# Performance work log

Measured on AMD Instinct MI355X. Metric: run time of the kernel, lower is better.

## Reference

```python
import jax, jax.numpy as jnp
import numpy as np

N = 20000      # nodes
E = 320000     # edges (avg degree 16)
DIN, H1, H2, DOUT = 256, 256, 128, 64


def _lin_params(key, din, dout):
    kw, kb = jax.random.split(key)
    s = 1.0 / np.sqrt(din)
    W = jax.random.uniform(kw, (din, dout), jnp.float32, -s, s)
    b = jax.random.uniform(kb, (dout,), jnp.float32, -s, s)
    return W, b


def setup_inputs() -> dict:
    key = jax.random.key(0)
    keys = jax.random.split(key, 20)
    inp = {
        'x': jax.random.normal(keys[0], (N, DIN), jnp.float32),
        'edge_index': jax.random.randint(keys[1], (2, E), 0, N, jnp.int64),
    }
    dims = [(DIN, H1), (DIN, H1), (DIN, H1),   # layer1 key/query/value
            (H1, H2), (H1, H2), (H1, H2),      # layer2
            (H2, DOUT), (H2, DOUT), (H2, DOUT)]  # layer3
    names = ['k1', 'q1', 'v1', 'k2', 'q2', 'v2', 'k3', 'q3', 'v3']
    for i, (nm, (di, do)) in enumerate(zip(names, dims)):
        W, b = _lin_params(keys[2 + i], di, do)
        inp[nm + '_w'] = W
        inp[nm + '_b'] = b
    # skip (root) weights, no bias per PyG, plus per-conv output bias
    for j, (di, do) in enumerate([(DIN, H1), (H1, H2), (H2, DOUT)], start=1):
        s = 1.0 / np.sqrt(di)
        inp[f's{j}_w'] = jax.random.uniform(keys[11 + 2 * j], (di, do), jnp.float32, -s, s)
        inp[f'bias{j}'] = jnp.zeros((do,), jnp.float32)
    return inp


def _res_gated_conv(x, src, dst, kw, kb, qw, qb, vw, vb, sw, bias):
    # PyG ResGatedGraphConv (flow source_to_target, aggr='add', act=Sigmoid):
    # out_i = lin_skip(x_i) + sum_{j->i} sigmoid(lin_key(x_i) + lin_query(x_j)) * lin_value(x_j) + bias
    k = x @ kw + kb            # [N, D]
    q = x @ qw + qb
    v = x @ vw + vb
    eta = jax.nn.sigmoid(k[dst] + q[src])   # [E, D] edge gate
    msg = eta * v[src]                      # [E, D]
    agg = jax.ops.segment_sum(msg, dst, num_segments=N)  # scatter-add to targets
    return x @ sw + agg + bias


def reference(x, edge_index,
              k1_w, k1_b, q1_w, q1_b, v1_w, v1_b,
              k2_w, k2_b, q2_w, q2_b, v2_w, v2_b,
              k3_w, k3_b, q3_w, q3_b, v3_w, v3_b,
              s1_w, bias1, s2_w, bias2, s3_w, bias3):
    src, dst = edge_index[0], edge_index[1]
    h = _res_gated_conv(x, src, dst, k1_w, k1_b, q1_w, q1_b, v1_w, v1_b, s1_w, bias1)
    # dropout (eval mode -> identity)
    h = _res_gated_conv(h, src, dst, k2_w, k2_b, q2_w, q2_b, v2_w, v2_b, s2_w, bias2)
    h = _res_gated_conv(h, src, dst, k3_w, k3_b, q3_w, q3_b, v3_w, v3_b, s3_w, bias3)
    return jax.nn.softmax(h, axis=1)
```

## Files before the change

### kernel.cpp

```cpp
#include <hip/hip_runtime.h>
#include <hip/hip_bf16.h>
#include <type_traits>


#define NN 20000
#define EE 320000
#define ELLW 64

typedef _Float16 half8 __attribute__((ext_vector_type(8)));
typedef _Float16 half4 __attribute__((ext_vector_type(4)));
typedef _Float16 half2v __attribute__((ext_vector_type(2)));
typedef float f32x4 __attribute__((ext_vector_type(4)));

__device__ __forceinline__ _Float16 f2h(float f) { return (_Float16)f; }
__device__ __forceinline__ float fsigmoid_mul(float v, float x) {
    return v * __builtin_amdgcn_rcpf(1.f + __expf(-x));
}

struct PrepArgs {
    const float* w[3][4];
    const float* b[3][4];
    _Float16* wt[3];
    float* cb[3];
};

__global__ __launch_bounds__(256) void setup_all_kernel(
    const int* __restrict__ ei, int* __restrict__ deg, int* __restrict__ flag,
    const float* __restrict__ x, _Float16* __restrict__ Xh, PrepArgs a) {
    const int b = blockIdx.x;
    const int tid = threadIdx.x;
    if (b < 79) {
        const int i = b * 256 + tid;
        if (i < NN) deg[i] = 0;
    } else if (b == 79) {
        __shared__ int nz;
        if (tid == 0) nz = 0;
        __syncthreads();
        int c = 0;
        for (int t = tid; t < 1024; t += 256)
            if (ei[2 * t + 1] != 0) c = 1;
        if (c) atomicAdd(&nz, 1);
        __syncthreads();
        if (tid == 0) *flag = (nz == 0) ? 1 : 0;
    } else if (b < 1744) {
        const int idx = (b - 80) * 256 + tid;
        int layer, li, K, D;
        if (idx < 262144) {
            layer = 0; li = idx; K = 256; D = 256;
        } else if (idx < 393216) {
            layer = 1; li = idx - 262144; K = 256; D = 128;
        } else {
            layer = 2; li = idx - 393216; K = 128; D = 64;
        }
        const int p = li / K;
        const int k = li - p * K;
        int grp, c;
        if (p < D) {
            grp = 0; c = p;
        } else if (p < 3 * D) {
            const int t = p - D;
            grp = (t & 1) ? 2 : 1;
            c = t >> 1;
        } else {
            grp = 3; c = p - 3 * D;
        }
        a.wt[layer][(size_t)p * K + k] =
            f2h(a.w[layer][grp][(size_t)k * D + c]);
        if (k == 0) a.cb[layer][p] = a.b[layer][grp][c];
    } else {
        const int i = ((b - 1744) * 256 + tid) * 8;
        if (i < NN * 256) {
            const float4 f0 = *(const float4*)(x + i);
            const float4 f1 = *(const float4*)(x + i + 4);
            half8 h;
            h[0] = f2h(f0.x); h[1] = f2h(f0.y); h[2] = f2h(f0.z); h[3] = f2h(f0.w);
            h[4] = f2h(f1.x); h[5] = f2h(f1.y); h[6] = f2h(f1.z); h[7] = f2h(f1.w);
            *(half8*)(Xh + i) = h;
        }
    }
}

__device__ __forceinline__ void gemm_tile(
    int bm, int bn, const _Float16* __restrict__ A,
    const _Float16* __restrict__ Bt, const float* __restrict__ catbias,
    _Float16* __restrict__ O, int M, int K, int N) {
    __shared__ _Float16 As[2][4096];
    __shared__ _Float16 Bs[2][4096];

    const int tid = threadIdx.x;
    const int wid = tid >> 6;
    const int lane = tid & 63;
    const int tile_m = bm * 128;
    const int tile_n = bn * 128;
    const int wm = (wid & 1) * 64;
    const int wn = (wid >> 1) * 64;

    const int st_row = (wid << 4) + (lane >> 2);
    const int st_kc = (lane & 3) << 3;

    auto stage = [&](int buf, int kt) {
#pragma unroll
        for (int j = 0; j < 2; ++j) {
            int ar = tile_m + j * 64 + st_row;
            ar = ar < M ? ar : M - 1;
            const _Float16* ag = A + (size_t)ar * K + kt + st_kc;
            __builtin_amdgcn_global_load_lds(
                (const __attribute__((address_space(1))) unsigned int*)ag,
                (__attribute__((address_space(3))) unsigned int*)
                    &As[buf][j * 2048 + (wid << 9)],
                16, 0, 0);
            const int br = tile_n + j * 64 + st_row;
            const _Float16* bg = Bt + (size_t)br * K + kt + st_kc;
            __builtin_amdgcn_global_load_lds(
                (const __attribute__((address_space(1))) unsigned int*)bg,
                (__attribute__((address_space(3))) unsigned int*)
                    &Bs[buf][j * 2048 + (wid << 9)],
                16, 0, 0);
        }
    };

    stage(0, 0);

    f32x4 acc[4][4] = {};
    const int fr = lane & 15;
    const int fk = (lane >> 4) << 3;
    const int niter = K >> 5;

    for (int it = 0; it < niter; ++it) {
        __syncthreads();
        if (it + 1 < niter) stage((it + 1) & 1, (it + 1) << 5);
        const _Float16* as = As[it & 1];
        const _Float16* bs = Bs[it & 1];
        half8 af[4], bf[4];
#pragma unroll
        for (int mi = 0; mi < 4; ++mi)
            af[mi] = *(const half8*)&as[(wm + mi * 16 + fr) * 32 + fk];
#pragma unroll
        for (int ni = 0; ni < 4; ++ni)
            bf[ni] = *(const half8*)&bs[(wn + ni * 16 + fr) * 32 + fk];
#pragma unroll
        for (int mi = 0; mi < 4; ++mi)
#pragma unroll
            for (int ni = 0; ni < 4; ++ni)
                acc[mi][ni] = __builtin_amdgcn_mfma_f32_16x16x32_f16(
                    af[mi], bf[ni], acc[mi][ni], 0, 0, 0);
    }
    __syncthreads();

    _Float16* zone = &As[0][0] + wid * 2048;
    const int cl = lane & 15;
    const int rq = (lane >> 4) << 2;
    const int col0 = tile_n + wn;
    const int r0 = tile_m + wm;
#pragma unroll
    for (int mi = 0; mi < 4; ++mi) {
#pragma unroll
        for (int ni = 0; ni < 4; ++ni) {
            const float cb = catbias[col0 + ni * 16 + cl];
#pragma unroll
            for (int r = 0; r < 4; ++r)
                zone[(rq + r) * 72 + ni * 16 + cl] = f2h(acc[mi][ni][r] + cb);
        }
#pragma unroll
        for (int j = 0; j < 2; ++j) {
            const int rr = j * 8 + (lane >> 3);
            const int row = r0 + mi * 16 + rr;
            const half8 v = *(const half8*)&zone[rr * 72 + (lane & 7) * 8];
            if (row < M)
                *(half8*)&O[(size_t)row * N + col0 + (lane & 7) * 8] = v;
        }
    }
}

__global__ __launch_bounds__(256) void gemm_kernel(
    const _Float16* __restrict__ A, const _Float16* __restrict__ Bt,
    const float* __restrict__ catbias, _Float16* __restrict__ O, int M, int K,
    int N, int mblocks) {
    gemm_tile(blockIdx.x % mblocks, blockIdx.x / mblocks, A, Bt, catbias, O, M,
              K, N);
}

__global__ __launch_bounds__(256) void gemm1_fill_kernel(
    const _Float16* __restrict__ A, const _Float16* __restrict__ Bt,
    const float* __restrict__ catbias, _Float16* __restrict__ O,
    const int* __restrict__ ei, const int* __restrict__ i64flag,
    int* __restrict__ deg, unsigned short* __restrict__ col) {
    if (blockIdx.x < 1256) {
        gemm_tile(blockIdx.x % 157, blockIdx.x / 157, A, Bt, catbias, O, NN,
                  256, 1024);
        return;
    }
    const int e = (blockIdx.x - 1256) * 256 + threadIdx.x;
    if (e >= EE) return;
    int src, dst;
    if (*i64flag) {
        const long long* p = (const long long*)ei;
        src = (int)p[e];
        dst = (int)p[EE + e];
    } else {
        src = ei[e];
        dst = ei[EE + e];
    }
    const int pos = atomicAdd(&deg[dst], 1);
    if (pos < ELLW) col[dst * ELLW + pos] = (unsigned short)src;
}

template <int D>
__global__ __launch_bounds__(256) void edge_gather_slice_kernel(
    const int* __restrict__ deg, const unsigned short* __restrict__ col,
    const _Float16* __restrict__ KQVS, _Float16* __restrict__ Hh, int n) {
    constexpr int NSL = D / 32;
    constexpr int D4 = 4 * D;
    const int b = blockIdx.x;
    const int s = b % NSL;
    const int g = b / NSL;
    const int node = g * 4 + (threadIdx.x >> 6);
    if (node >= n) return;
    const int lane = threadIdx.x & 63;
    const int d = lane & 31;
    const int esub = lane >> 5;

    int dg = deg[node];
    dg = dg < ELLW ? dg : ELLW;
    int idx = (int)col[node * ELLW + lane];
    if (lane >= dg) idx = node;

    const int el = s * 32 + d;
    const float k = (float)KQVS[(size_t)node * D4 + el];
    const _Float16* qv = KQVS + D + 2 * el;
    float acc = 0.f;

    for (int e = 0; e < dg; e += 4) {
        const int s0 = __shfl(idx, e + esub, 64);
        const int s1 = __shfl(idx, e + 2 + esub, 64);
        const half2v u0 = *(const half2v*)(qv + (size_t)s0 * D4);
        const half2v u1 = *(const half2v*)(qv + (size_t)s1 * D4);
        const float g0 = fsigmoid_mul((float)u0[1], k + (float)u0[0]);
        acc += (e + esub < dg) ? g0 : 0.f;
        const float g1 = fsigmoid_mul((float)u1[1], k + (float)u1[0]);
        acc += (e + 2 + esub < dg) ? g1 : 0.f;
    }
    acc += __shfl_xor(acc, 32, 64);

    if (lane < 32) {
        const float skip = (float)KQVS[(size_t)node * D4 + 3 * D + el];
        Hh[(size_t)node * D + el] = f2h(skip + acc);
    }
}

template <int D, int MODE>
__global__ __launch_bounds__(256, 4) void edge_gather_kernel(
    const int* __restrict__ deg, const unsigned short* __restrict__ col,
    const _Float16* __restrict__ KQVS, _Float16* __restrict__ Hh,
    float* __restrict__ out, int n) {
    constexpr int DV = D / 64;
    constexpr int D4 = 4 * D;
    using qv_t = typename std::conditional<
        DV == 4, half8,
        typename std::conditional<DV == 2, half4, half2v>::type>::type;

    const int node = blockIdx.x * 4 + (threadIdx.x >> 6);
    if (node >= n) return;
    const int lane = threadIdx.x & 63;
    const int ld = lane * DV;

    int dg = deg[node];
    dg = dg < ELLW ? dg : ELLW;
    int idx = (int)col[node * ELLW + lane];
    if (lane >= dg) idx = node;

    float k[DV], acc[DV];
    {
        const _Float16* kp = KQVS + (size_t)node * D4 + ld;
        if constexpr (DV == 4) {
            const half4 u = *(const half4*)kp;
#pragma unroll
            for (int j = 0; j < 4; ++j) k[j] = (float)u[j];
        } else if constexpr (DV == 2) {
            const half2v u = *(const half2v*)kp;
            k[0] = (float)u[0]; k[1] = (float)u[1];
        } else {
            k[0] = (float)*kp;
        }
    }
#pragma unroll
    for (int j = 0; j < DV; ++j) acc[j] = 0.f;

    auto ldqv = [&](qv_t& u, int e) {
        const int s = __builtin_amdgcn_readlane(idx, e);
        const qv_t* p = (const qv_t*)(KQVS + (size_t)s * D4 + D) + lane;
        u = *p;
    };
    auto edgeacc = [&](qv_t u) {
#pragma unroll
        for (int j = 0; j < DV; ++j)
            acc[j] += fsigmoid_mul((float)u[2 * j + 1], k[j] + (float)u[2 * j]);
    };

    qv_t ua[8], ub[8];
    auto issue = [&](qv_t* u, int e0) {
#pragma unroll
        for (int j = 0; j < 8; ++j) ldqv(u[j], e0 + j);
    };
    auto consume8 = [&](qv_t* u) {
#pragma unroll
        for (int j = 0; j < 8; ++j) edgeacc(u[j]);
    };
    auto consume_tail = [&](qv_t* u, int nb) {
#pragma unroll
        for (int j = 0; j < 8; ++j)
            if (j < nb) edgeacc(u[j]);
    };

    if (dg > 0) {
        issue(ua, 0);
        for (int e = 0;;) {
            int nb = dg - e;
            if (nb <= 8) {
                __builtin_amdgcn_sched_barrier(0);
                consume_tail(ua, nb);
                break;
            }
            issue(ub, e + 8);
            __builtin_amdgcn_sched_barrier(0);
            consume8(ua);
            e += 8;
            nb = dg - e;
            if (nb <= 8) {
                __builtin_amdgcn_sched_barrier(0);
                consume_tail(ub, nb);
                break;
            }
            issue(ua, e + 8);
            __builtin_amdgcn_sched_barrier(0);
            consume8(ub);
            e += 8;
        }
    }

    float h[DV];
    {
        const _Float16* sp = KQVS + (size_t)node * D4 + 3 * D + ld;
        if constexpr (DV == 4) {
            const half4 u = *(const half4*)sp;
#pragma unroll
            for (int j = 0; j < 4; ++j) h[j] = (float)u[j] + acc[j];
        } else if constexpr (DV == 2) {
            const half2v u = *(const half2v*)sp;
            h[0] = (float)u[0] + acc[0];
            h[1] = (float)u[1] + acc[1];
        } else {
            h[0] = (float)*sp + acc[0];
        }
    }

    if constexpr (MODE == 0) {
        _Float16* op = Hh + (size_t)node * D + ld;
        if constexpr (DV == 4) {
            half4 o;
#pragma unroll
            for (int j = 0; j < 4; ++j) o[j] = f2h(h[j]);
            *(half4*)op = o;
        } else if constexpr (DV == 2) {
            half2v o;
            o[0] = f2h(h[0]); o[1] = f2h(h[1]);
            *(half2v*)op = o;
        } else {
            op[0] = f2h(h[0]);
        }
    } else {
        static_assert(MODE == 0 || DV == 1, "softmax fusion needs D==64");
        float m = h[0];
#pragma unroll
        for (int off = 32; off > 0; off >>= 1)
            m = fmaxf(m, __shfl_xor(m, off, 64));
        const float ex = __expf(h[0] - m);
        float sm = ex;
#pragma unroll
        for (int off = 32; off > 0; off >>= 1) sm += __shfl_xor(sm, off, 64);
        out[(size_t)node * 64 + lane] = ex * __builtin_amdgcn_rcpf(sm);
    }
}

extern "C" void kernel_launch(void* const* d_in, const int* in_sizes, int n_in,
                              void* d_out, int out_size, void* d_ws,
                              size_t ws_size, hipStream_t stream) {
    const float* x = (const float*)d_in[0];
    const int* ei = (const int*)d_in[1];

    char* w = (char*)d_ws;
    _Float16* Xh = (_Float16*)w;     w += (size_t)NN * 256 * 2;
    _Float16* KQVS = (_Float16*)w;   w += (size_t)NN * 1024 * 2;
    _Float16* H1h = (_Float16*)w;    w += (size_t)NN * 256 * 2;
    _Float16* H2h = (_Float16*)w;    w += (size_t)NN * 128 * 2;
    _Float16* Wt1 = (_Float16*)w;    w += (size_t)1024 * 256 * 2;
    _Float16* Wt2 = (_Float16*)w;    w += (size_t)512 * 256 * 2;
    _Float16* Wt3 = (_Float16*)w;    w += (size_t)256 * 128 * 2;
    float* cb1 = (float*)w;          w += 1024 * 4;
    float* cb2 = (float*)w;          w += 512 * 4;
    float* cb3 = (float*)w;          w += 256 * 4;
    int* i64flag = (int*)w;          w += 16;
    int* deg = (int*)w;              w += (size_t)NN * 4;
    unsigned short* ell = (unsigned short*)w;  w += (size_t)NN * ELLW * 2;

    const dim3 blk(256);
    const int gblocks = (NN + 3) / 4;

    PrepArgs pa;
    pa.w[0][0] = (const float*)d_in[2];  pa.b[0][0] = (const float*)d_in[3];
    pa.w[0][1] = (const float*)d_in[4];  pa.b[0][1] = (const float*)d_in[5];
    pa.w[0][2] = (const float*)d_in[6];  pa.b[0][2] = (const float*)d_in[7];
    pa.w[1][0] = (const float*)d_in[8];  pa.b[1][0] = (const float*)d_in[9];
    pa.w[1][1] = (const float*)d_in[10]; pa.b[1][1] = (const float*)d_in[11];
    pa.w[1][2] = (const float*)d_in[12]; pa.b[1][2] = (const float*)d_in[13];
    pa.w[2][0] = (const float*)d_in[14]; pa.b[2][0] = (const float*)d_in[15];
    pa.w[2][1] = (const float*)d_in[16]; pa.b[2][1] = (const float*)d_in[17];
    pa.w[2][2] = (const float*)d_in[18]; pa.b[2][2] = (const float*)d_in[19];
    pa.w[0][3] = (const float*)d_in[20]; pa.b[0][3] = (const float*)d_in[21];
    pa.w[1][3] = (const float*)d_in[22]; pa.b[1][3] = (const float*)d_in[23];
    pa.w[2][3] = (const float*)d_in[24]; pa.b[2][3] = (const float*)d_in[25];
    pa.wt[0] = Wt1; pa.wt[1] = Wt2; pa.wt[2] = Wt3;
    pa.cb[0] = cb1; pa.cb[1] = cb2; pa.cb[2] = cb3;

    setup_all_kernel<<<4244, blk, 0, stream>>>(ei, deg, i64flag, x, Xh, pa);

    gemm1_fill_kernel<<<2506, blk, 0, stream>>>(Xh, Wt1, cb1, KQVS, ei,
                                                i64flag, deg, ell);
    edge_gather_slice_kernel<256><<<gblocks * 8, blk, 0, stream>>>(
        deg, ell, KQVS, H1h, NN);

    gemm_kernel<<<157 * 4, blk, 0, stream>>>(H1h, Wt2, cb2, KQVS, NN, 256, 512,
                                             157);
    edge_gather_slice_kernel<128><<<gblocks * 4, blk, 0, stream>>>(
        deg, ell, KQVS, H2h, NN);

    gemm_kernel<<<157 * 2, blk, 0, stream>>>(H2h, Wt3, cb3, KQVS, NN, 128, 256,
                                             157);
    edge_gather_kernel<64, 1><<<gblocks, blk, 0, stream>>>(
        deg, ell, KQVS, nullptr, (float*)d_out, NN);
}
```

Measured before the change: 287.2 us.

## Reorganize q/v weight interleave and vectorize sliced edge gather with fp16 exp

```diff
diff --git a/kernel.cpp b/kernel.cpp
--- a/kernel.cpp
+++ b/kernel.cpp
@@ -15,6 +15,11 @@
 __device__ __forceinline__ _Float16 f2h(float f) { return (_Float16)f; }
 __device__ __forceinline__ float fsigmoid_mul(float v, float x) {
     return v * __builtin_amdgcn_rcpf(1.f + __expf(-x));
+}
+__device__ __forceinline__ _Float16 h_exp2(_Float16 x) {
+    _Float16 r;
+    asm("v_exp_f16 %0, %1" : "=v"(r) : "v"(x));
+    return r;
 }
 
 struct PrepArgs {
@@ -59,8 +64,14 @@
             grp = 0; c = p;
         } else if (p < 3 * D) {
             const int t = p - D;
-            grp = (t & 1) ? 2 : 1;
-            c = t >> 1;
+            if (layer < 2) {
+                const int pb = t >> 2, r = t & 3;
+                grp = (r < 2) ? 1 : 2;
+                c = 2 * pb + (r & 1);
+            } else {
+                grp = (t & 1) ? 2 : 1;
+                c = t >> 1;
+            }
         } else {
             grp = 3; c = p - 3 * D;
         }
@@ -212,39 +223,111 @@
     constexpr int NSL = D / 32;
     constexpr int D4 = 4 * D;
     const int b = blockIdx.x;
-    const int s = b % NSL;
+    const int sl = b % NSL;
     const int g = b / NSL;
     const int node = g * 4 + (threadIdx.x >> 6);
     if (node >= n) return;
     const int lane = threadIdx.x & 63;
-    const int d = lane & 31;
-    const int esub = lane >> 5;
+    const int d = lane & 7;
+    const int esub = lane >> 3;
 
     int dg = deg[node];
     dg = dg < ELLW ? dg : ELLW;
     int idx = (int)col[node * ELLW + lane];
     if (lane >= dg) idx = node;
 
-    const int el = s * 32 + d;
-    const float k = (float)KQVS[(size_t)node * D4 + el];
-    const _Float16* qv = KQVS + D + 2 * el;
-    float acc = 0.f;
-
-    for (int e = 0; e < dg; e += 4) {
-        const int s0 = __shfl(idx, e + esub, 64);
-        const int s1 = __shfl(idx, e + 2 + esub, 64);
-        const half2v u0 = *(const half2v*)(qv + (size_t)s0 * D4);
-        const half2v u1 = *(const half2v*)(qv + (size_t)s1 * D4);
-        const float g0 = fsigmoid_mul((float)u0[1], k + (float)u0[0]);
-        acc += (e + esub < dg) ? g0 : 0.f;
-        const float g1 = fsigmoid_mul((float)u1[1], k + (float)u1[0]);
-        acc += (e + 2 + esub < dg) ? g1 : 0.f;
-    }
-    acc += __shfl_xor(acc, 32, 64);
-
-    if (lane < 32) {
-        const float skip = (float)KQVS[(size_t)node * D4 + 3 * D + el];
-        Hh[(size_t)node * D + el] = f2h(skip + acc);
+    const half2v mlg = {(_Float16)-1.44269504f, (_Float16)-1.44269504f};
+    const half4 kq =
+        *(const half4*)(KQVS + (size_t)node * D4 + sl * 32 + d * 4);
+    const half2v mk01 = half2v{kq[0], kq[1]} * mlg;
+    const half2v mk23 = half2v{kq[2], kq[3]} * mlg;
+
+    float acc0 = 0.f, acc1 = 0.f, acc2 = 0.f, acc3 = 0.f;
+
+    const _Float16* qv0 = KQVS + D + 64 * sl + 8 * d;
+
+    auto ldqv = [&](half8& u, int e0) {
+        const int s = __shfl(idx, e0 + esub, 64);
+        u = *(const half8*)(qv0 + ((size_t)s << (D == 256 ? 10 : 9)));
+    };
+    auto gate = [&](half8 u, float& g0, float& g1, float& g2, float& g3) {
+        const half2v mt01 = half2v{u[0], u[1]} * mlg + mk01;
+        const half2v mt23 = half2v{u[4], u[5]} * mlg + mk23;
+        const float e0 = (float)h_exp2(mt01[0]);
+        const float e1 = (float)h_exp2(mt01[1]);
+        const float e2 = (float)h_exp2(mt23[0]);
+        const float e3 = (float)h_exp2(mt23[1]);
+        const float r0 = __builtin_amdgcn_rcpf(1.f + e0);
+        const float r1 = __builtin_amdgcn_rcpf(1.f + e1);
+        const float r2 = __builtin_amdgcn_rcpf(1.f + e2);
+        const float r3 = __builtin_amdgcn_rcpf(1.f + e3);
+        g0 = r0 * (float)u[2];
+        g1 = r1 * (float)u[3];
+        g2 = r2 * (float)u[6];
+        g3 = r3 * (float)u[7];
+    };
+    auto consume8 = [&](half8 u) {
+        float g0, g1, g2, g3;
+        gate(u, g0, g1, g2, g3);
+        acc0 += g0; acc1 += g1; acc2 += g2; acc3 += g3;
+    };
+    auto consume_tail = [&](half8 u, int nb) {
+        const float msk = (esub < nb) ? 1.f : 0.f;
+        float g0, g1, g2, g3;
+        gate(u, g0, g1, g2, g3);
+        acc0 += msk * g0; acc1 += msk * g1;
+        acc2 += msk * g2; acc3 += msk * g3;
+    };
+
+    if (dg > 0) {
+        half8 ua, ub;
+        ldqv(ua, 0);
+        for (int e = 0;;) {
+            int nb = dg - e;
+            if (nb <= 8) {
+                __builtin_amdgcn_sched_barrier(0);
+                consume_tail(ua, nb);
+                break;
+            }
+            ldqv(ub, e + 8);
+            __builtin_amdgcn_sched_barrier(0);
+            consume8(ua);
+            e += 8;
+            nb = dg - e;
+            if (nb <= 8) {
+                __builtin_amdgcn_sched_barrier(0);
+                consume_tail(ub, nb);
+                break;
+            }
+            ldqv(ua, e + 8);
+            __builtin_amdgcn_sched_barrier(0);
+            consume8(ub);
+            e += 8;
+        }
+    }
+
+    acc0 += __shfl_xor(acc0, 8, 64);
+    acc0 += __shfl_xor(acc0, 16, 64);
+    acc0 += __shfl_xor(acc0, 32, 64);
+    acc1 += __shfl_xor(acc1, 8, 64);
+    acc1 += __shfl_xor(acc1, 16, 64);
+    acc1 += __shfl_xor(acc1, 32, 64);
+    acc2 += __shfl_xor(acc2, 8, 64);
+    acc2 += __shfl_xor(acc2, 16, 64);
+    acc2 += __shfl_xor(acc2, 32, 64);
+    acc3 += __shfl_xor(acc3, 8, 64);
+    acc3 += __shfl_xor(acc3, 16, 64);
+    acc3 += __shfl_xor(acc3, 32, 64);
+
+    if (esub == 0) {
+        const half4 sv =
+            *(const half4*)(KQVS + (size_t)node * D4 + 3 * D + sl * 32 + d * 4);
+        half4 o;
+        o[0] = f2h((float)sv[0] + acc0);
+        o[1] = f2h((float)sv[1] + acc1);
+        o[2] = f2h((float)sv[2] + acc2);
+        o[3] = f2h((float)sv[3] + acc3);
+        *(half4*)(Hh + (size_t)node * D + sl * 32 + d * 4) = o;
     }
 }
 
```

Result: faster. 275.9 us (-3.9%).

## Interleave KQVS columns per 32-feature slice and pipeline slice gathers

Applied to the files above, without the earlier changes.

```diff
diff --git a/kernel.cpp b/kernel.cpp
--- a/kernel.cpp
+++ b/kernel.cpp
@@ -54,15 +54,17 @@
         }
         const int p = li / K;
         const int k = li - p * K;
+        const int sl = p >> 7;
+        const int r = p & 127;
         int grp, c;
-        if (p < D) {
-            grp = 0; c = p;
-        } else if (p < 3 * D) {
-            const int t = p - D;
+        if (r < 32) {
+            grp = 0; c = sl * 32 + r;
+        } else if (r < 96) {
+            const int t = r - 32;
             grp = (t & 1) ? 2 : 1;
-            c = t >> 1;
+            c = sl * 32 + (t >> 1);
         } else {
-            grp = 3; c = p - 3 * D;
+            grp = 3; c = sl * 32 + (r - 96);
         }
         a.wt[layer][(size_t)p * K + k] =
             f2h(a.w[layer][grp][(size_t)k * D + c]);
@@ -206,107 +208,126 @@
 }
 
 template <int D>
-__global__ __launch_bounds__(256) void edge_gather_slice_kernel(
+__global__ __launch_bounds__(256, 4) void slice_gather_kernel(
     const int* __restrict__ deg, const unsigned short* __restrict__ col,
     const _Float16* __restrict__ KQVS, _Float16* __restrict__ Hh, int n) {
     constexpr int NSL = D / 32;
     constexpr int D4 = 4 * D;
     const int b = blockIdx.x;
-    const int s = b % NSL;
-    const int g = b / NSL;
-    const int node = g * 4 + (threadIdx.x >> 6);
+    const int sl = b % NSL;
+    const int node = (b / NSL) * 4 + (threadIdx.x >> 6);
     if (node >= n) return;
     const int lane = threadIdx.x & 63;
-    const int d = lane & 31;
-    const int esub = lane >> 5;
+    const int fl = lane & 31;
+    const int eh = lane >> 5;
 
     int dg = deg[node];
     dg = dg < ELLW ? dg : ELLW;
     int idx = (int)col[node * ELLW + lane];
     if (lane >= dg) idx = node;
 
-    const int el = s * 32 + d;
-    const float k = (float)KQVS[(size_t)node * D4 + el];
-    const _Float16* qv = KQVS + D + 2 * el;
+    const _Float16* chunk_n = KQVS + (size_t)node * D4 + sl * 128;
+    const float k = (float)chunk_n[fl];
     float acc = 0.f;
 
-    for (int e = 0; e < dg; e += 4) {
-        const int s0 = __shfl(idx, e + esub, 64);
-        const int s1 = __shfl(idx, e + 2 + esub, 64);
-        const half2v u0 = *(const half2v*)(qv + (size_t)s0 * D4);
-        const half2v u1 = *(const half2v*)(qv + (size_t)s1 * D4);
-        const float g0 = fsigmoid_mul((float)u0[1], k + (float)u0[0]);
-        acc += (e + esub < dg) ? g0 : 0.f;
-        const float g1 = fsigmoid_mul((float)u1[1], k + (float)u1[0]);
-        acc += (e + 2 + esub < dg) ? g1 : 0.f;
-    }
+    auto ldqv = [&](half2v& u, int e2) {
+        const int sA = __builtin_amdgcn_readlane(idx, e2);
+        const int sB = __builtin_amdgcn_readlane(idx, e2 + 1);
+        const int s = (lane < 32) ? sA : sB;
+        u = *((const half2v*)(KQVS + (size_t)s * D4 + sl * 128 + 32) + fl);
+    };
+    auto edgeacc = [&](half2v u, float m) {
+        acc += m * fsigmoid_mul((float)u[1], k + (float)u[0]);
+    };
+
+    half2v ua[4], ub[4];
+    auto issue = [&](half2v* u, int e0) {
+#pragma unroll
+        for (int i = 0; i < 4; ++i) ldqv(u[i], e0 + 2 * i);
+    };
+    auto consume4 = [&](half2v* u) {
+#pragma unroll
+        for (int i = 0; i < 4; ++i) edgeacc(u[i], 1.f);
+    };
+    auto consume_tail = [&](half2v* u, int nb) {
+#pragma unroll
+        for (int i = 0; i < 4; ++i) {
+            const float m = (2 * i + eh < nb) ? 1.f : 0.f;
+            edgeacc(u[i], m);
+        }
+    };
+
+    if (dg > 0) {
+        issue(ua, 0);
+        for (int e = 0;;) {
+            int nb = dg - e;
+            if (nb <= 8) {
+                __builtin_amdgcn_sched_barrier(0);
+                consume_tail(ua, nb);
+                break;
+            }
+            issue(ub, e + 8);
+            __builtin_amdgcn_sched_barrier(0);
+            consume4(ua);
+            e += 8;
+            nb = dg - e;
+            if (nb <= 8) {
+                __builtin_amdgcn_sched_barrier(0);
+                consume_tail(ub, nb);
+                break;
+            }
+            issue(ua, e + 8);
+            __builtin_amdgcn_sched_barrier(0);
+            consume4(ub);
+            e += 8;
+        }
+    }
+
     acc += __shfl_xor(acc, 32, 64);
 
     if (lane < 32) {
-        const float skip = (float)KQVS[(size_t)node * D4 + 3 * D + el];
-        Hh[(size_t)node * D + el] = f2h(skip + acc);
-    }
-}
-
-template <int D, int MODE>
-__global__ __launch_bounds__(256, 4) void edge_gather_kernel(
+        const float skip = (float)chunk_n[96 + fl];
+        Hh[(size_t)node * D + sl * 32 + fl] = f2h(skip + acc);
+    }
+}
+
+__global__ __launch_bounds__(256, 4) void gather64_softmax_kernel(
     const int* __restrict__ deg, const unsigned short* __restrict__ col,
-    const _Float16* __restrict__ KQVS, _Float16* __restrict__ Hh,
-    float* __restrict__ out, int n) {
-    constexpr int DV = D / 64;
-    constexpr int D4 = 4 * D;
-    using qv_t = typename std::conditional<
-        DV == 4, half8,
-        typename std::conditional<DV == 2, half4, half2v>::type>::type;
-
+    const _Float16* __restrict__ KQVS, float* __restrict__ out, int n) {
     const int node = blockIdx.x * 4 + (threadIdx.x >> 6);
     if (node >= n) return;
     const int lane = threadIdx.x & 63;
-    const int ld = lane * DV;
+    const int sl = lane >> 5;
+    const int fo = lane & 31;
+    const int qvoff = sl * 128 + 32 + 2 * fo;
 
     int dg = deg[node];
     dg = dg < ELLW ? dg : ELLW;
     int idx = (int)col[node * ELLW + lane];
     if (lane >= dg) idx = node;
 
-    float k[DV], acc[DV];
-    {
-        const _Float16* kp = KQVS + (size_t)node * D4 + ld;
-        if constexpr (DV == 4) {
-            const half4 u = *(const half4*)kp;
-#pragma unroll
-            for (int j = 0; j < 4; ++j) k[j] = (float)u[j];
-        } else if constexpr (DV == 2) {
-            const half2v u = *(const half2v*)kp;
-            k[0] = (float)u[0]; k[1] = (float)u[1];
-        } else {
-            k[0] = (float)*kp;
-        }
-    }
-#pragma unroll
-    for (int j = 0; j < DV; ++j) acc[j] = 0.f;
-
-    auto ldqv = [&](qv_t& u, int e) {
+    const _Float16* chunk_n = KQVS + (size_t)node * 256 + sl * 128;
+    const float k = (float)chunk_n[fo];
+    float acc = 0.f;
+
+    auto ldqv = [&](half2v& u, int e) {
         const int s = __builtin_amdgcn_readlane(idx, e);
-        const qv_t* p = (const qv_t*)(KQVS + (size_t)s * D4 + D) + lane;
-        u = *p;
-    };
-    auto edgeacc = [&](qv_t u) {
-#pragma unroll
-        for (int j = 0; j < DV; ++j)
-            acc[j] += fsigmoid_mul((float)u[2 * j + 1], k[j] + (float)u[2 * j]);
-    };
-
-    qv_t ua[8], ub[8];
-    auto issue = [&](qv_t* u, int e0) {
+        u = *(const half2v*)(KQVS + (size_t)s * 256 + qvoff);
+    };
+    auto edgeacc = [&](half2v u) {
+        acc += fsigmoid_mul((float)u[1], k + (float)u[0]);
+    };
+
+    half2v ua[8], ub[8];
+    auto issue = [&](half2v* u, int e0) {
 #pragma unroll
         for (int j = 0; j < 8; ++j) ldqv(u[j], e0 + j);
     };
-    auto consume8 = [&](qv_t* u) {
+    auto consume8 = [&](half2v* u) {
 #pragma unroll
         for (int j = 0; j < 8; ++j) edgeacc(u[j]);
     };
-    auto consume_tail = [&](qv_t* u, int nb) {
+    auto consume_tail = [&](half2v* u, int nb) {
 #pragma unroll
         for (int j = 0; j < 8; ++j)
             if (j < nb) edgeacc(u[j]);
@@ -338,48 +359,17 @@
         }
     }
 
-    float h[DV];
-    {
-        const _Float16* sp = KQVS + (size_t)node * D4 + 3 * D + ld;
-        if constexpr (DV == 4) {
-            const half4 u = *(const half4*)sp;
-#pragma unroll
-            for (int j = 0; j < 4; ++j) h[j] = (float)u[j] + acc[j];
-        } else if constexpr (DV == 2) {
-            const half2v u = *(const half2v*)sp;
-            h[0] = (float)u[0] + acc[0];
-            h[1] = (float)u[1] + acc[1];
-        } else {
-            h[0] = (float)*sp + acc[0];
-        }
-    }
-
-    if constexpr (MODE == 0) {
-        _Float16* op = Hh + (size_t)node * D + ld;
-        if constexpr (DV == 4) {
-            half4 o;
-#pragma unroll
-            for (int j = 0; j < 4; ++j) o[j] = f2h(h[j]);
-            *(half4*)op = o;
-        } else if constexpr (DV == 2) {
-            half2v o;
-            o[0] = f2h(h[0]); o[1] = f2h(h[1]);
-            *(half2v*)op = o;
-        } else {
-            op[0] = f2h(h[0]);
-        }
-    } else {
-        static_assert(MODE == 0 || DV == 1, "softmax fusion needs D==64");
-        float m = h[0];
-#pragma unroll
-        for (int off = 32; off > 0; off >>= 1)
-            m = fmaxf(m, __shfl_xor(m, off, 64));
-        const float ex = __expf(h[0] - m);
-        float sm = ex;
-#pragma unroll
-        for (int off = 32; off > 0; off >>= 1) sm += __shfl_xor(sm, off, 64);
-        out[(size_t)node * 64 + lane] = ex * __builtin_amdgcn_rcpf(sm);
-    }
+    const float h = (float)chunk_n[96 + fo] + acc;
+
+    float m = h;
+#pragma unroll
+    for (int off = 32; off > 0; off >>= 1)
+        m = fmaxf(m, __shfl_xor(m, off, 64));
+    const float ex = __expf(h - m);
+    float sm = ex;
+#pragma unroll
+    for (int off = 32; off > 0; off >>= 1) sm += __shfl_xor(sm, off, 64);
+    out[(size_t)node * 64 + lane] = ex * __builtin_amdgcn_rcpf(sm);
 }
 
 extern "C" void kernel_launch(void* const* d_in, const int* in_sizes, int n_in,
@@ -426,16 +416,16 @@
 
     gemm1_fill_kernel<<<2506, blk, 0, stream>>>(Xh, Wt1, cb1, KQVS, ei,
                                                 i64flag, deg, ell);
-    edge_gather_slice_kernel<256><<<gblocks * 8, blk, 0, stream>>>(
+    slice_gather_kernel<256><<<gblocks * 8, blk, 0, stream>>>(
         deg, ell, KQVS, H1h, NN);
 
     gemm_kernel<<<157 * 4, blk, 0, stream>>>(H1h, Wt2, cb2, KQVS, NN, 256, 512,
                                              157);
-    edge_gather_slice_kernel<128><<<gblocks * 4, blk, 0, stream>>>(
+    slice_gather_kernel<128><<<gblocks * 4, blk, 0, stream>>>(
         deg, ell, KQVS, H2h, NN);
 
     gemm_kernel<<<157 * 2, blk, 0, stream>>>(H2h, Wt3, cb3, KQVS, NN, 128, 256,
                                              157);
-    edge_gather_kernel<64, 1><<<gblocks, blk, 0, stream>>>(
-        deg, ell, KQVS, nullptr, (float*)d_out, NN);
-}
+    gather64_softmax_kernel<<<gblocks, blk, 0, stream>>>(
+        deg, ell, KQVS, (float*)d_out, NN);
+}
```

Result: slower. 299.7 us (+4.3%).
